# Performance work log

Hardware: AMD Instinct MI355X
Metric: run time of the kernel (lower is better)

Reference implementation:

```python
import jax, jax.numpy as jnp
import numpy as np

B, N, C = 64, 8192, 64
C4 = C // 4
EPS_BN = 1e-5


def setup_inputs() -> dict:
    key = jax.random.key(0)
    ks = jax.random.split(key, 12)
    s = 0.05
    return {
        "x": jax.random.normal(ks[0], (B, N, 10), jnp.float32),
        "y": jax.random.normal(ks[1], (B, N, 13), jnp.float32),
        "W_l": jax.random.normal(ks[2], (10, C), jnp.float32) * s,
        "b_l": jax.random.normal(ks[3], (C,), jnp.float32) * s,
        "W_r": jax.random.normal(ks[4], (13, C), jnp.float32) * s,
        "b_r": jax.random.normal(ks[5], (C,), jnp.float32) * s,
        "W_qk": jax.random.normal(ks[6], (C4, C), jnp.float32) * s,  # shared q/k 1x1-conv weight
        "W_v": jax.random.normal(ks[7], (C, C), jnp.float32) * s,
        "b_v": jax.random.normal(ks[8], (C,), jnp.float32) * s,
        "W_t": jax.random.normal(ks[9], (C, C), jnp.float32) * s,
        "b_t": jax.random.normal(ks[10], (C,), jnp.float32) * s,
        "gamma": jnp.ones((C,), jnp.float32),
        "beta": jnp.zeros((C,), jnp.float32),
    }


def reference(x, y, W_l, b_l, W_r, b_r, W_qk, W_v, b_v, W_t, b_t, gamma, beta):
    # x: [B,N,10] -> linear_l; y: [B,N,13] -> linear_r  (torch keeps [B,C,N]; we keep [B,N,C])
    X = x @ W_l + b_l                                   # [B,N,C]
    Y = y @ W_r + b_r                                   # [B,N,C]
    # 1x1 convs == per-point matmuls; attention runs ACROSS the batch dim per point n
    xq = jnp.einsum('bnc,dc->nbd', X, W_qk)             # [N,B,C/4]
    yk = jnp.einsum('bnc,dc->nbd', Y, W_qk)             # [N,B,C/4] (shared weight)
    yv = jnp.einsum('bnc,dc->nbd', Y, W_v) + b_v        # [N,B,C]
    energy = jnp.einsum('nbd,ned->nbe', xq, yk)         # [N,B,B]
    attn = jax.nn.softmax(energy, axis=-1)
    # extra L1 renormalization over dim=1 (offset-attention style)
    attn = attn / (1e-9 + attn.sum(axis=1, keepdims=True))
    yr = jnp.einsum('nbe,nec->bnc', attn, yv)           # [B,N,C]
    # trans_conv -> BatchNorm (training-mode batch stats) -> ReLU -> residual -> max over points
    t = jnp.einsum('bnc,dc->bnd', X - yr, W_t) + b_t    # [B,N,C]
    mean = t.mean(axis=(0, 1))
    var = t.var(axis=(0, 1))                            # biased var, as BN uses
    tn = gamma * (t - mean) * jax.lax.rsqrt(var + EPS_BN) + beta
    xres = X + jax.nn.relu(tn)                          # [B,N,C]
    return jnp.max(xres, axis=1)[:, :, None]            # [B,C,1] to match torch layout
```

## Files before the change

kernel.cpp:

```cpp
#include <hip/hip_runtime.h>

#define B_ 64
#define N_ 8192

using short8 = __attribute__((ext_vector_type(8))) short;
using f32x4  = __attribute__((ext_vector_type(4))) float;

#define MFMA16(a, b, c) __builtin_amdgcn_mfma_f32_16x16x32_bf16((a), (b), (c), 0, 0, 0)

__device__ inline unsigned short f2bf(float f) {
  union { float f; unsigned int u; } v; v.f = f;
  return (unsigned short)((v.u + 0x8000u) >> 16);
}
__device__ inline float bf2f(unsigned int hi16_in_low) {
  union { unsigned int u; float f; } v; v.u = hi16_in_low << 16;
  return v.f;
}


__global__ void k0_prep(const float* __restrict__ W_l, const float* __restrict__ b_l,
                        const float* __restrict__ W_r, const float* __restrict__ b_r,
                        const float* __restrict__ W_qk, const float* __restrict__ W_v,
                        const float* __restrict__ b_v, const float* __restrict__ W_t,
                        float* __restrict__ wsf) {
  const int tid = threadIdx.x;
  unsigned short* wb   = (unsigned short*)(wsf + 66688);
  unsigned short* BM   = wb;
  unsigned short* BL   = wb + 512;
  unsigned short* BRV2 = wb + 2560;
  unsigned short* BT   = wb + 4608;
  if (blockIdx.x == 0) {
    __shared__ float Wlq[11 * 16], Wrk[14 * 16];
    for (int idx = tid; idx < 11 * 16; idx += 256) {
      int i = idx >> 4, d = idx & 15;
      const float* a = (i < 10) ? (W_l + i * 64) : b_l;
      float s = 0.f;
      for (int c = 0; c < 64; ++c) s = fmaf(a[c], W_qk[d * 64 + c], s);
      Wlq[idx] = s;
    }
    for (int idx = tid; idx < 14 * 16; idx += 256) {
      int j = idx >> 4, d = idx & 15;
      const float* a = (j < 13) ? (W_r + j * 64) : b_r;
      float s = 0.f;
      for (int c = 0; c < 64; ++c) s = fmaf(a[c], W_qk[d * 64 + c], s);
      Wrk[idx] = s;
    }
    __syncthreads();
    for (int idx = tid; idx < 512; idx += 256) {
      int j = idx >> 5, kk = idx & 31;
      unsigned short o = 0;
      if (j < 14 && kk < 11) {
        float s = 0.f;
        for (int d = 0; d < 16; ++d) s = fmaf(Wlq[kk * 16 + d], Wrk[j * 16 + d], s);
        o = f2bf(s);
      }
      BM[idx] = o;
    }
  } else if (blockIdx.x == 1) {
    for (int idx = tid; idx < 2048; idx += 256) {
      int c = idx >> 5, kk = idx & 31;
      unsigned short o = 0;
      if (kk < 13) {
        float s = 0.f;
        for (int j = 0; j < 64; ++j) s = fmaf(W_r[kk * 64 + j], W_v[c * 64 + j], s);
        o = f2bf(s);
      } else if (kk == 13) {
        float s = b_v[c];
        for (int j = 0; j < 64; ++j) s = fmaf(b_r[j], W_v[c * 64 + j], s);
        o = f2bf(s);
      }
      BRV2[idx] = o;
    }
  } else if (blockIdx.x == 2) {
    for (int idx = tid; idx < 2048; idx += 256) {
      int c = idx >> 5, kk = idx & 31;
      unsigned short o = 0;
      if (kk < 10) o = f2bf(W_l[kk * 64 + c]);
      else if (kk == 10) o = f2bf(b_l[c]);
      BL[idx] = o;
    }
    for (int i = tid; i < 1024; i += 256) wsf[i] = 0.f;
  } else {
    for (int i = tid; i < 4096; i += 256) BT[i] = f2bf(W_t[i]);
  }
}

__global__ __launch_bounds__(256, 4)
void k1_attn(const float* __restrict__ x, const float* __restrict__ y,
             const float* __restrict__ wsf, const float* __restrict__ b_t,
             float* __restrict__ stats) {
  __shared__ __align__(16) short lds[18688];
  float* const scr = (float*)lds;
  short* const Axy[2] = {lds, lds + 2560};
  short* const YTb[2] = {lds + 5120, lds + 6272};
  short* const awB    = lds + 7424;
  short* const guB    = lds + 16640;

  const unsigned short* wb   = (const unsigned short*)(wsf + 66688);
  const unsigned short* BM   = wb;
  const unsigned short* BL   = wb + 512;
  const unsigned short* BRV2 = wb + 2560;
  const unsigned short* BT   = wb + 4608;
  unsigned short* tg = (unsigned short*)(wsf + 66688) + 8704;

  const int tid  = threadIdx.x;
  const int w    = tid >> 6;
  const int lane = tid & 63;
  const int l15  = lane & 15;
  const int q    = lane >> 4;
  const int r0   = w * 16;
  const int n0   = blockIdx.x * 2;
  short* const aw[2] = {awB + w * 1152, awB + (4 + w) * 1152};
  short* const gu[2] = {guB + w * 256,  guB + (4 + w) * 256};

  {
    const int b = tid >> 2, i = tid & 3;
#pragma unroll
    for (int p = 0; p < 2; ++p) {
      const float* xp = x + ((size_t)b * N_ + n0 + p) * 10;
      const float* yp = y + ((size_t)b * N_ + n0 + p) * 13;
      short* Ar = Axy[p] + b * 40;
      Ar[i]     = (short)f2bf(xp[i]);
      Ar[i + 4] = (short)f2bf(xp[i + 4]);
      short v8 = 0;
      if (i < 2) v8 = (short)f2bf(xp[i + 8]);
      else if (i == 2) v8 = (short)0x3F80;
      Ar[i + 8]  = v8;
      Ar[i + 12] = 0;
      const short y0 = (short)f2bf(yp[i]);
      const short y1 = (short)f2bf(yp[i + 4]);
      const short y2 = (short)f2bf(yp[i + 8]);
      short y3 = 0;
      if (i == 0) y3 = (short)f2bf(yp[12]);
      else if (i == 1) y3 = (short)0x3F80;
      Ar[16 + i] = y0;  Ar[20 + i] = y1;  Ar[24 + i] = y2;  Ar[28 + i] = y3;
      short* YT = YTb[p];
      YT[i * 72 + b] = y0;  YT[(i + 4) * 72 + b] = y1;
      YT[(i + 8) * 72 + b] = y2;  YT[(i + 12) * 72 + b] = y3;
    }
  }
  __syncthreads();

  const short8 z8 = {0, 0, 0, 0, 0, 0, 0, 0};
  const f32x4 zero4 = {0.f, 0.f, 0.f, 0.f};

  const short8 bmF = *(const short8*)&BM[l15 * 32 + q * 8];
  short8 blF[4];
#pragma unroll
  for (int f = 0; f < 4; ++f) blF[f] = *(const short8*)&BL[(f * 16 + l15) * 32 + q * 8];

  f32x4 X[2][4];
#pragma unroll
  for (int p = 0; p < 2; ++p) {
    const short8 aA = *(const short8*)&Axy[p][(r0 + l15) * 40 + q * 8];
    f32x4 G = MFMA16(aA, bmF, zero4);
#pragma unroll
    for (int f = 0; f < 4; ++f) X[p][f] = MFMA16(aA, blF[f], zero4);
#pragma unroll
    for (int j = 0; j < 4; ++j) gu[p][(q * 4 + j) * 16 + l15] = (short)f2bf(G[j]);
  }

  f32x4 E[2][4];
#pragma unroll
  for (int p = 0; p < 2; ++p) {
    short8 aG = z8;
    if (q < 2) aG = *(const short8*)&gu[p][l15 * 16 + q * 8];
#pragma unroll
    for (int f = 0; f < 4; ++f) {
      short8 bk = z8;
      if (q < 2) bk = *(const short8*)&Axy[p][(f * 16 + l15) * 40 + 16 + q * 8];
      E[p][f] = MFMA16(aG, bk, zero4);
    }
  }
  __syncthreads();

  float inv_r[2][4];
#pragma unroll
  for (int p = 0; p < 2; ++p)
#pragma unroll
    for (int j = 0; j < 4; ++j) {
      float s = 0.f;
#pragma unroll
      for (int f = 0; f < 4; ++f) { E[p][f][j] = __expf(E[p][f][j]); s += E[p][f][j]; }
      s += __shfl_xor(s, 1);
      s += __shfl_xor(s, 2);
      s += __shfl_xor(s, 4);
      s += __shfl_xor(s, 8);
      inv_r[p][j] = 1.0f / s;
    }
#pragma unroll
  for (int p = 0; p < 2; ++p)
#pragma unroll
    for (int f = 0; f < 4; ++f) {
      float cs = E[p][f][0] * inv_r[p][0] + E[p][f][1] * inv_r[p][1] +
                 E[p][f][2] * inv_r[p][2] + E[p][f][3] * inv_r[p][3];
      cs += __shfl_xor(cs, 16);
      cs += __shfl_xor(cs, 32);
      if (lane < 16) scr[p * 256 + w * 64 + f * 16 + l15] = cs;
    }
  __syncthreads();

#pragma unroll
  for (int p = 0; p < 2; ++p) {
#pragma unroll
    for (int f = 0; f < 4; ++f) {
      const int col = f * 16 + l15;
      const float* sp = scr + p * 256;
      const float csv = 1.0f / (1e-9f + sp[col] + sp[64 + col] + sp[128 + col] + sp[192 + col]);
#pragma unroll
      for (int j = 0; j < 4; ++j)
        aw[p][(q * 4 + j) * 72 + col] = (short)f2bf(E[p][f][j] * inv_r[p][j] * csv);
    }
  }

  short8 brvF[4];
#pragma unroll
  for (int f = 0; f < 4; ++f) brvF[f] = *(const short8*)&BRV2[(f * 16 + l15) * 32 + q * 8];
#pragma unroll
  for (int p = 0; p < 2; ++p) {
    const short8 aA0 = *(const short8*)&aw[p][l15 * 72 + q * 8];
    const short8 aA1 = *(const short8*)&aw[p][l15 * 72 + 32 + q * 8];
    f32x4 U = MFMA16(aA0, *(const short8*)&YTb[p][l15 * 72 + q * 8], zero4);
    U = MFMA16(aA1, *(const short8*)&YTb[p][l15 * 72 + 32 + q * 8], U);
#pragma unroll
    for (int j = 0; j < 4; ++j) gu[p][(q * 4 + j) * 16 + l15] = (short)f2bf(U[j]);
    short8 aU = z8;
    if (q < 2) aU = *(const short8*)&gu[p][l15 * 16 + q * 8];
#pragma unroll
    for (int f = 0; f < 4; ++f) {
      f32x4 yr = MFMA16(aU, brvF[f], zero4);
#pragma unroll
      for (int j = 0; j < 4; ++j)
        aw[p][(q * 4 + j) * 72 + f * 16 + l15] = (short)f2bf(X[p][f][j] - yr[j]);
    }
  }

  f32x4 t[2][4];
  float sRed[2][4], ssRed[2][4];
  uint2 pk[2][4];
  float4 btv[4];
#pragma unroll
  for (int f = 0; f < 4; ++f) btv[f] = *(const float4*)&b_t[f * 16 + q * 4];
#pragma unroll
  for (int p = 0; p < 2; ++p) {
    const short8 aZ0 = *(const short8*)&aw[p][l15 * 72 + q * 8];
    const short8 aZ1 = *(const short8*)&aw[p][l15 * 72 + 32 + q * 8];
#pragma unroll
    for (int f = 0; f < 4; ++f) {
      const int c = f * 16 + l15;
      const float bT = b_t[c];
      const short8 bt0 = *(const short8*)&BT[c * 64 + q * 8];
      const short8 bt1 = *(const short8*)&BT[c * 64 + 32 + q * 8];
      t[p][f] = MFMA16(aZ0, bt0, ((f32x4){bT, bT, bT, bT}));
      t[p][f] = MFMA16(aZ1, bt1, t[p][f]);
      float s = 0.f, ss = 0.f;
#pragma unroll
      for (int j = 0; j < 4; ++j) { s += t[p][f][j]; ss = fmaf(t[p][f][j], t[p][f][j], ss); }
      s  += __shfl_xor(s, 16);  s  += __shfl_xor(s, 32);
      ss += __shfl_xor(ss, 16); ss += __shfl_xor(ss, 32);
      sRed[p][f] = s; ssRed[p][f] = ss;
      f32x4 tc = MFMA16(bt0, aZ0, ((f32x4){btv[f].x, btv[f].y, btv[f].z, btv[f].w}));
      tc = MFMA16(bt1, aZ1, tc);
      pk[p][f].x = (unsigned)f2bf(tc[0]) | ((unsigned)f2bf(tc[1]) << 16);
      pk[p][f].y = (unsigned)f2bf(tc[2]) | ((unsigned)f2bf(tc[3]) << 16);
    }
  }
  __syncthreads();
#pragma unroll
  for (int p = 0; p < 2; ++p)
#pragma unroll
    for (int f = 0; f < 4; ++f)
      if (lane < 16) {
        scr[p * 512 + w * 64 + f * 16 + l15]       = sRed[p][f];
        scr[p * 512 + 256 + w * 64 + f * 16 + l15] = ssRed[p][f];
      }
  __syncthreads();
  if (tid < 128) {
    const int p = tid >> 6, c = tid & 63;
    const float* sp = scr + p * 512;
    const float s  = sp[c] + sp[64 + c] + sp[128 + c] + sp[192 + c];
    const float ss = sp[256 + c] + sp[320 + c] + sp[384 + c] + sp[448 + c];
    float* st = stats + ((n0 + p) & 7) * 128;
    atomicAdd(&st[c], s);
    atomicAdd(&st[64 + c], ss);
  }
#pragma unroll
  for (int p = 0; p < 2; ++p)
#pragma unroll
    for (int f = 0; f < 4; ++f)
      *(uint2*)&tg[(size_t)(n0 + p) * 4096 + (size_t)(r0 + l15) * 64 + f * 16 + q * 4] =
          pk[p][f];
}

__global__ void k2_stats(const float* __restrict__ stats, float* __restrict__ meanr) {
  const int c = threadIdx.x;
  if (c < 64) {
    float s = 0.f, ss = 0.f;
    for (int r = 0; r < 8; ++r) { s += stats[r * 128 + c]; ss += stats[r * 128 + 64 + c]; }
    const float inv = 1.0f / (float)(B_ * N_);
    const float mu = s * inv;
    const float var = fmaf(ss, inv, -mu * mu);
    meanr[c] = mu;
    meanr[64 + c] = rsqrtf(var + 1e-5f);
  }
}

__global__ __launch_bounds__(256)
void k3_max(const float* __restrict__ x, const float* __restrict__ W_l,
            const float* __restrict__ b_l, const float* __restrict__ gamma,
            const float* __restrict__ beta, const unsigned short* __restrict__ tg,
            const float* __restrict__ meanr, float* __restrict__ pmax)
{
  const int b = blockIdx.x >> 4;
  const int chunk = blockIdx.x & 15;
  const int wv = threadIdx.x >> 6;
  const int lane = threadIdx.x & 63;
  const int c0 = (lane & 15) * 4;
  const int nsub = lane >> 4;
  float4 wl4[10];
#pragma unroll
  for (int k = 0; k < 10; ++k) wl4[k] = *(const float4*)&W_l[k * 64 + c0];
  const float4 bl  = *(const float4*)&b_l[c0];
  const float4 g   = *(const float4*)&gamma[c0];
  const float4 be  = *(const float4*)&beta[c0];
  const float4 mu  = *(const float4*)&meanr[c0];
  const float4 rs  = *(const float4*)&meanr[64 + c0];
  float4 grs, bmb;
  grs.x = g.x * rs.x; grs.y = g.y * rs.y; grs.z = g.z * rs.z; grs.w = g.w * rs.w;
  bmb.x = be.x - mu.x * grs.x; bmb.y = be.y - mu.y * grs.y;
  bmb.z = be.z - mu.z * grs.z; bmb.w = be.w - mu.w * grs.w;
  float4 m = {-1e30f, -1e30f, -1e30f, -1e30f};
  const int n0 = chunk * 512 + wv * 128 + nsub;
  for (int jj = 0; jj < 32; ++jj) {
    const int n = n0 + jj * 4;
    const uint2 tv = *(const uint2*)&tg[(size_t)n * 4096 + (b << 6) + c0];
    const float* xp = x + ((size_t)b * N_ + n) * 10;
    float4 X = bl;
#pragma unroll
    for (int k = 0; k < 10; ++k) {
      const float xk = xp[k];
      X.x = fmaf(xk, wl4[k].x, X.x); X.y = fmaf(xk, wl4[k].y, X.y);
      X.z = fmaf(xk, wl4[k].z, X.z); X.w = fmaf(xk, wl4[k].w, X.w);
    }
    const float t0 = bf2f(tv.x & 0xFFFFu), t1 = bf2f(tv.x >> 16);
    const float t2 = bf2f(tv.y & 0xFFFFu), t3 = bf2f(tv.y >> 16);
    m.x = fmaxf(m.x, X.x + fmaxf(fmaf(t0, grs.x, bmb.x), 0.f));
    m.y = fmaxf(m.y, X.y + fmaxf(fmaf(t1, grs.y, bmb.y), 0.f));
    m.z = fmaxf(m.z, X.z + fmaxf(fmaf(t2, grs.z, bmb.z), 0.f));
    m.w = fmaxf(m.w, X.w + fmaxf(fmaf(t3, grs.w, bmb.w), 0.f));
  }
  m.x = fmaxf(m.x, __shfl_xor(m.x, 16)); m.y = fmaxf(m.y, __shfl_xor(m.y, 16));
  m.z = fmaxf(m.z, __shfl_xor(m.z, 16)); m.w = fmaxf(m.w, __shfl_xor(m.w, 16));
  m.x = fmaxf(m.x, __shfl_xor(m.x, 32)); m.y = fmaxf(m.y, __shfl_xor(m.y, 32));
  m.z = fmaxf(m.z, __shfl_xor(m.z, 32)); m.w = fmaxf(m.w, __shfl_xor(m.w, 32));
  __shared__ float sm[4][64];
  if (lane < 16) *(float4*)&sm[wv][c0] = m;
  __syncthreads();
  if (threadIdx.x < 64) {
    const float r = fmaxf(fmaxf(sm[0][threadIdx.x], sm[1][threadIdx.x]),
                          fmaxf(sm[2][threadIdx.x], sm[3][threadIdx.x]));
    pmax[(size_t)blockIdx.x * 64 + threadIdx.x] = r;
  }
}

__global__ void k4_final(const float* __restrict__ pmax, float* __restrict__ out) {
  const int b = blockIdx.x, c = threadIdx.x;
  float m = -1e30f;
  for (int ch = 0; ch < 16; ++ch) m = fmaxf(m, pmax[((size_t)b * 16 + ch) * 64 + c]);
  out[b * 64 + c] = m;
}

extern "C" void kernel_launch(void* const* d_in, const int* in_sizes, int n_in,
                              void* d_out, int out_size, void* d_ws, size_t ws_size,
                              hipStream_t stream) {
  const float* x     = (const float*)d_in[0];
  const float* y     = (const float*)d_in[1];
  const float* W_l   = (const float*)d_in[2];
  const float* b_l   = (const float*)d_in[3];
  const float* W_r   = (const float*)d_in[4];
  const float* b_r   = (const float*)d_in[5];
  const float* W_qk  = (const float*)d_in[6];
  const float* W_v   = (const float*)d_in[7];
  const float* b_v   = (const float*)d_in[8];
  const float* W_t   = (const float*)d_in[9];
  const float* b_t   = (const float*)d_in[10];
  const float* gamma = (const float*)d_in[11];
  const float* beta  = (const float*)d_in[12];
  float* out = (float*)d_out;

  float* wsf = (float*)d_ws;
  float* stats = wsf;
  float* meanr = wsf + 1024;
  float* pmax  = wsf + 1152;
  const unsigned short* tg = (const unsigned short*)(wsf + 66688) + 8704;

  hipLaunchKernelGGL(k0_prep, dim3(4), dim3(256), 0, stream,
                     W_l, b_l, W_r, b_r, W_qk, W_v, b_v, W_t, wsf);
  hipLaunchKernelGGL(k1_attn, dim3(N_ / 2), dim3(256), 0, stream,
                     x, y, wsf, b_t, stats);
  hipLaunchKernelGGL(k2_stats, dim3(1), dim3(64), 0, stream, stats, meanr);
  hipLaunchKernelGGL(k3_max, dim3(1024), dim3(256), 0, stream,
                     x, W_l, b_l, gamma, beta, tg, meanr, pmax);
  hipLaunchKernelGGL(k4_final, dim3(64), dim3(64), 0, stream, pmax, out);
}
```

Before: 205.1 us.

## Vectorize attention input staging, add MFMA priority hints, fold stats kernel into max pass

```diff
diff --git a/kernel.cpp b/kernel.cpp
--- a/kernel.cpp
+++ b/kernel.cpp
@@ -15,6 +15,14 @@
 __device__ inline float bf2f(unsigned int hi16_in_low) {
   union { unsigned int u; float f; } v; v.u = hi16_in_low << 16;
   return v.f;
+}
+__device__ inline unsigned u2(float a, float b) {
+  return (unsigned)f2bf(a) | ((unsigned)f2bf(b) << 16);
+}
+__device__ inline void put_y(short* Ar0, short* YT0, int b, int f, unsigned short h) {
+  const int s = (f >= 13) ? 1 : 0;
+  Ar0[16 + f + 2547 * s] = (short)h;
+  YT0[f * 72 + b + 216 * s] = (short)h;
 }
 
 
@@ -115,31 +123,48 @@
 
   {
     const int b = tid >> 2, i = tid & 3;
-#pragma unroll
-    for (int p = 0; p < 2; ++p) {
-      const float* xp = x + ((size_t)b * N_ + n0 + p) * 10;
-      const float* yp = y + ((size_t)b * N_ + n0 + p) * 13;
-      short* Ar = Axy[p] + b * 40;
-      Ar[i]     = (short)f2bf(xp[i]);
-      Ar[i + 4] = (short)f2bf(xp[i + 4]);
-      short v8 = 0;
-      if (i < 2) v8 = (short)f2bf(xp[i + 8]);
-      else if (i == 2) v8 = (short)0x3F80;
-      Ar[i + 8]  = v8;
-      Ar[i + 12] = 0;
-      const short y0 = (short)f2bf(yp[i]);
-      const short y1 = (short)f2bf(yp[i + 4]);
-      const short y2 = (short)f2bf(yp[i + 8]);
-      short y3 = 0;
-      if (i == 0) y3 = (short)f2bf(yp[12]);
-      else if (i == 1) y3 = (short)0x3F80;
-      Ar[16 + i] = y0;  Ar[20 + i] = y1;  Ar[24 + i] = y2;  Ar[28 + i] = y3;
-      short* YT = YTb[p];
-      YT[i * 72 + b] = y0;  YT[(i + 4) * 72 + b] = y1;
-      YT[(i + 8) * 72 + b] = y2;  YT[(i + 12) * 72 + b] = y3;
-    }
-  }
-  __syncthreads();
+    const float* xb = x + ((size_t)b * N_ + n0) * 10;
+    const float* yb = y + ((size_t)b * N_ + n0) * 13;
+    short* const Ar0 = Axy[0] + b * 40;
+    short* const Ar1 = Axy[1] + b * 40;
+    short* const YT0 = YTb[0];
+    {
+      const float4 v = *(const float4*)(xb + 4 * i);
+      const int g0 = 4 * i, g1 = 4 * i + 2;
+      *(unsigned*)(Ar0 + (g0 >= 10 ? g0 + 2550 : g0)) = u2(v.x, v.y);
+      *(unsigned*)(Ar0 + (g1 >= 10 ? g1 + 2550 : g1)) = u2(v.z, v.w);
+      if (i == 0) {
+        const float4 vv = *(const float4*)(xb + 16);
+        *(unsigned*)(Ar1 + 6) = u2(vv.x, vv.y);
+        *(unsigned*)(Ar1 + 8) = u2(vv.z, vv.w);
+      }
+    }
+    if (i == 1) { *(unsigned*)(Ar1 + 10) = 0x3F80u; *(unsigned*)(Ar1 + 12) = 0u; *(unsigned*)(Ar1 + 14) = 0u; }
+    if (i == 2) { *(unsigned*)(Ar0 + 10) = 0x3F80u; *(unsigned*)(Ar0 + 12) = 0u; *(unsigned*)(Ar0 + 14) = 0u; }
+#pragma unroll
+    for (int t = 0; t < 3; ++t) {
+      const int j = i + 4 * t;
+      const float2 v = *(const float2*)(yb + 2 * j);
+      put_y(Ar0, YT0, b, 2 * j,     f2bf(v.x));
+      put_y(Ar0, YT0, b, 2 * j + 1, f2bf(v.y));
+    }
+    if (i == 0) {
+      const float2 v = *(const float2*)(yb + 24);
+      put_y(Ar0, YT0, b, 24, f2bf(v.x));
+      put_y(Ar0, YT0, b, 25, f2bf(v.y));
+    }
+    if (i == 3) {
+      Ar0[29] = (short)0x3F80; *(unsigned*)(Ar0 + 30) = 0u;
+      YT0[13 * 72 + b] = (short)0x3F80; YT0[14 * 72 + b] = 0; YT0[15 * 72 + b] = 0;
+    }
+    if (i == 2) {
+      Ar1[29] = (short)0x3F80; *(unsigned*)(Ar1 + 30) = 0u;
+      short* YT1 = YT0 + 1152;
+      YT1[13 * 72 + b] = (short)0x3F80; YT1[14 * 72 + b] = 0; YT1[15 * 72 + b] = 0;
+    }
+  }
+  asm volatile("s_waitcnt lgkmcnt(0)" ::: "memory");
+  __builtin_amdgcn_sched_barrier(0);
 
   const short8 z8 = {0, 0, 0, 0, 0, 0, 0, 0};
   const f32x4 zero4 = {0.f, 0.f, 0.f, 0.f};
@@ -150,6 +175,7 @@
   for (int f = 0; f < 4; ++f) blF[f] = *(const short8*)&BL[(f * 16 + l15) * 32 + q * 8];
 
   f32x4 X[2][4];
+  __builtin_amdgcn_s_setprio(1);
 #pragma unroll
   for (int p = 0; p < 2; ++p) {
     const short8 aA = *(const short8*)&Axy[p][(r0 + l15) * 40 + q * 8];
@@ -159,8 +185,11 @@
 #pragma unroll
     for (int j = 0; j < 4; ++j) gu[p][(q * 4 + j) * 16 + l15] = (short)f2bf(G[j]);
   }
+  __builtin_amdgcn_s_setprio(0);
+  __syncthreads();
 
   f32x4 E[2][4];
+  __builtin_amdgcn_s_setprio(1);
 #pragma unroll
   for (int p = 0; p < 2; ++p) {
     short8 aG = z8;
@@ -172,6 +201,7 @@
       E[p][f] = MFMA16(aG, bk, zero4);
     }
   }
+  __builtin_amdgcn_s_setprio(0);
   __syncthreads();
 
   float inv_r[2][4];
@@ -216,6 +246,7 @@
   short8 brvF[4];
 #pragma unroll
   for (int f = 0; f < 4; ++f) brvF[f] = *(const short8*)&BRV2[(f * 16 + l15) * 32 + q * 8];
+  __builtin_amdgcn_s_setprio(1);
 #pragma unroll
   for (int p = 0; p < 2; ++p) {
     const short8 aA0 = *(const short8*)&aw[p][l15 * 72 + q * 8];
@@ -234,6 +265,7 @@
         aw[p][(q * 4 + j) * 72 + f * 16 + l15] = (short)f2bf(X[p][f][j] - yr[j]);
     }
   }
+  __builtin_amdgcn_s_setprio(0);
 
   f32x4 t[2][4];
   float sRed[2][4], ssRed[2][4];
@@ -241,6 +273,7 @@
   float4 btv[4];
 #pragma unroll
   for (int f = 0; f < 4; ++f) btv[f] = *(const float4*)&b_t[f * 16 + q * 4];
+  __builtin_amdgcn_s_setprio(1);
 #pragma unroll
   for (int p = 0; p < 2; ++p) {
     const short8 aZ0 = *(const short8*)&aw[p][l15 * 72 + q * 8];
@@ -265,6 +298,7 @@
       pk[p][f].y = (unsigned)f2bf(tc[2]) | ((unsigned)f2bf(tc[3]) << 16);
     }
   }
+  __builtin_amdgcn_s_setprio(0);
   __syncthreads();
 #pragma unroll
   for (int p = 0; p < 2; ++p)
@@ -292,27 +326,33 @@
           pk[p][f];
 }
 
-__global__ void k2_stats(const float* __restrict__ stats, float* __restrict__ meanr) {
-  const int c = threadIdx.x;
-  if (c < 64) {
+__global__ __launch_bounds__(256)
+void k3_max(const float* __restrict__ x, const float* __restrict__ W_l,
+            const float* __restrict__ b_l, const float* __restrict__ gamma,
+            const float* __restrict__ beta, const unsigned short* __restrict__ tg,
+            const float* __restrict__ stats, float* __restrict__ pmax)
+{
+  const int b = blockIdx.x >> 4;
+  const int chunk = blockIdx.x & 15;
+  __shared__ __align__(16) float xs[512 * 10];
+  __shared__ float mr[128];
+  __shared__ float sm[4][64];
+  {
+    const float4* src = (const float4*)(x + ((size_t)b * N_ + (size_t)chunk * 512) * 10);
+    float4* dst = (float4*)xs;
+#pragma unroll
+    for (int t = 0; t < 5; ++t) dst[threadIdx.x + 256 * t] = src[threadIdx.x + 256 * t];
+  }
+  if (threadIdx.x < 64) {
+    const int c = threadIdx.x;
     float s = 0.f, ss = 0.f;
     for (int r = 0; r < 8; ++r) { s += stats[r * 128 + c]; ss += stats[r * 128 + 64 + c]; }
     const float inv = 1.0f / (float)(B_ * N_);
     const float mu = s * inv;
     const float var = fmaf(ss, inv, -mu * mu);
-    meanr[c] = mu;
-    meanr[64 + c] = rsqrtf(var + 1e-5f);
-  }
-}
-
-__global__ __launch_bounds__(256)
-void k3_max(const float* __restrict__ x, const float* __restrict__ W_l,
-            const float* __restrict__ b_l, const float* __restrict__ gamma,
-            const float* __restrict__ beta, const unsigned short* __restrict__ tg,
-            const float* __restrict__ meanr, float* __restrict__ pmax)
-{
-  const int b = blockIdx.x >> 4;
-  const int chunk = blockIdx.x & 15;
+    mr[c] = mu;
+    mr[64 + c] = rsqrtf(var + 1e-5f);
+  }
   const int wv = threadIdx.x >> 6;
   const int lane = threadIdx.x & 63;
   const int c0 = (lane & 15) * 4;
@@ -323,24 +363,28 @@
   const float4 bl  = *(const float4*)&b_l[c0];
   const float4 g   = *(const float4*)&gamma[c0];
   const float4 be  = *(const float4*)&beta[c0];
-  const float4 mu  = *(const float4*)&meanr[c0];
-  const float4 rs  = *(const float4*)&meanr[64 + c0];
+  __syncthreads();
+  const float4 mu  = *(const float4*)&mr[c0];
+  const float4 rs  = *(const float4*)&mr[64 + c0];
   float4 grs, bmb;
   grs.x = g.x * rs.x; grs.y = g.y * rs.y; grs.z = g.z * rs.z; grs.w = g.w * rs.w;
   bmb.x = be.x - mu.x * grs.x; bmb.y = be.y - mu.y * grs.y;
   bmb.z = be.z - mu.z * grs.z; bmb.w = be.w - mu.w * grs.w;
   float4 m = {-1e30f, -1e30f, -1e30f, -1e30f};
-  const int n0 = chunk * 512 + wv * 128 + nsub;
+  const int ln0 = wv * 128 + nsub;
+#pragma unroll 2
   for (int jj = 0; jj < 32; ++jj) {
-    const int n = n0 + jj * 4;
-    const uint2 tv = *(const uint2*)&tg[(size_t)n * 4096 + (b << 6) + c0];
-    const float* xp = x + ((size_t)b * N_ + n) * 10;
+    const int ln = ln0 + jj * 4;
+    const uint2 tv = *(const uint2*)&tg[(size_t)(chunk * 512 + ln) * 4096 + (b << 6) + c0];
+    const float2* xr = (const float2*)(xs + ln * 10);
     float4 X = bl;
 #pragma unroll
-    for (int k = 0; k < 10; ++k) {
-      const float xk = xp[k];
-      X.x = fmaf(xk, wl4[k].x, X.x); X.y = fmaf(xk, wl4[k].y, X.y);
-      X.z = fmaf(xk, wl4[k].z, X.z); X.w = fmaf(xk, wl4[k].w, X.w);
+    for (int k = 0; k < 5; ++k) {
+      const float2 xk = xr[k];
+      X.x = fmaf(xk.x, wl4[2 * k].x, X.x); X.y = fmaf(xk.x, wl4[2 * k].y, X.y);
+      X.z = fmaf(xk.x, wl4[2 * k].z, X.z); X.w = fmaf(xk.x, wl4[2 * k].w, X.w);
+      X.x = fmaf(xk.y, wl4[2 * k + 1].x, X.x); X.y = fmaf(xk.y, wl4[2 * k + 1].y, X.y);
+      X.z = fmaf(xk.y, wl4[2 * k + 1].z, X.z); X.w = fmaf(xk.y, wl4[2 * k + 1].w, X.w);
     }
     const float t0 = bf2f(tv.x & 0xFFFFu), t1 = bf2f(tv.x >> 16);
     const float t2 = bf2f(tv.y & 0xFFFFu), t3 = bf2f(tv.y >> 16);
@@ -353,7 +397,6 @@
   m.z = fmaxf(m.z, __shfl_xor(m.z, 16)); m.w = fmaxf(m.w, __shfl_xor(m.w, 16));
   m.x = fmaxf(m.x, __shfl_xor(m.x, 32)); m.y = fmaxf(m.y, __shfl_xor(m.y, 32));
   m.z = fmaxf(m.z, __shfl_xor(m.z, 32)); m.w = fmaxf(m.w, __shfl_xor(m.w, 32));
-  __shared__ float sm[4][64];
   if (lane < 16) *(float4*)&sm[wv][c0] = m;
   __syncthreads();
   if (threadIdx.x < 64) {
@@ -390,7 +433,6 @@
 
   float* wsf = (float*)d_ws;
   float* stats = wsf;
-  float* meanr = wsf + 1024;
   float* pmax  = wsf + 1152;
   const unsigned short* tg = (const unsigned short*)(wsf + 66688) + 8704;
 
@@ -398,8 +440,7 @@
                      W_l, b_l, W_r, b_r, W_qk, W_v, b_v, W_t, wsf);
   hipLaunchKernelGGL(k1_attn, dim3(N_ / 2), dim3(256), 0, stream,
                      x, y, wsf, b_t, stats);
-  hipLaunchKernelGGL(k2_stats, dim3(1), dim3(64), 0, stream, stats, meanr);
   hipLaunchKernelGGL(k3_max, dim3(1024), dim3(256), 0, stream,
-                     x, W_l, b_l, gamma, beta, tg, meanr, pmax);
+                     x, W_l, b_l, gamma, beta, tg, stats, pmax);
   hipLaunchKernelGGL(k4_final, dim3(64), dim3(64), 0, stream, pmax, out);
 }
```

Result: no change. 202.7 us (-1.2%).
